# Performance work log

Hardware: AMD Instinct MI355X
Metric: run time of the kernel (lower is better)

The kernel has to match this reference:

```python
import jax, jax.numpy as jnp
import numpy as np

D = 256
EXP = 4


def layer_norm(x, gamma, beta, eps=1e-5):
    mu = jnp.mean(x, axis=-1, keepdims=True)
    var = jnp.var(x, axis=-1, keepdims=True)
    return (x - mu) / jnp.sqrt(var + eps) * gamma + beta


def setup_inputs() -> dict:
    key = jax.random.key(0)
    ks = jax.random.split(key, 7)
    B, N = 8, 2048
    x = jax.random.normal(ks[0], (B, N, D), dtype=jnp.float32)
    w1 = jax.random.normal(ks[1], (D, EXP * D), dtype=jnp.float32) * (1.0 / np.sqrt(D))
    b1 = jnp.zeros((EXP * D,), dtype=jnp.float32)
    w2 = jax.random.normal(ks[2], (EXP * D, D), dtype=jnp.float32) * (1.0 / np.sqrt(EXP * D))
    b2 = jnp.zeros((D,), dtype=jnp.float32)
    g1 = jnp.ones((D,), dtype=jnp.float32)
    be1 = jnp.zeros((D,), dtype=jnp.float32)
    g2 = jnp.ones((D,), dtype=jnp.float32)
    be2 = jnp.zeros((D,), dtype=jnp.float32)
    return {"x": x, "w1": w1, "b1": b1, "w2": w2, "b2": b2,
            "gamma1": g1, "beta1": be1, "gamma2": g2, "beta2": be2}


def reference(x, w1, b1, w2, b2, gamma1, beta1, gamma2, beta2):
    # Sublayer 1: x + SA(LN(x)); SA uses raw QK^T softmax with Q=K=V=LN(x)
    h = layer_norm(x, gamma1, beta1)               # [B,N,D]
    scale = jnp.sqrt(jnp.float32(h.shape[-1]))
    scores = jnp.einsum('bnd,bmd->bnm', h, h) / scale  # [B,N,N]
    prob = jax.nn.softmax(scores, axis=-1)
    sa_out = jnp.einsum('bnm,bmd->bnd', prob, h)
    x = x + sa_out
    # Sublayer 2: x + FFN(LN(x))
    h2 = layer_norm(x, gamma2, beta2)
    ffn = jax.nn.relu(h2 @ w1 + b1) @ w2 + b2
    return x + ffn
```

## Files before the change

kernel.cpp:

```cpp
#include <hip/hip_runtime.h>
#include <hip/hip_bf16.h>

typedef unsigned short u16;
typedef __attribute__((ext_vector_type(8))) short short8;
typedef __attribute__((ext_vector_type(4))) float f32x4;

typedef unsigned int __attribute__((address_space(1))) as1_u32;
typedef unsigned int __attribute__((address_space(3))) as3_u32;

__device__ __forceinline__ void gload16(const void* g, void* l) {
    __builtin_amdgcn_global_load_lds((const as1_u32*)g, (as3_u32*)l, 16, 0, 0);
}

__device__ __forceinline__ u16 f2b(float f) {
    union { float f; unsigned u; } v; v.f = f;
    unsigned r = v.u + 0x7fffu + ((v.u >> 16) & 1u);
    return (u16)(r >> 16);
}

__global__ void transpose_cast(const float* __restrict__ src,
                               u16* __restrict__ dst, int R, int C) {
    __shared__ float tile[32][33];
    const int c0 = blockIdx.x * 32, r0 = blockIdx.y * 32;
    const int tx = threadIdx.x, ty = threadIdx.y;
#pragma unroll
    for (int i = ty; i < 32; i += 8)
        tile[i][tx] = src[(size_t)(r0 + i) * C + c0 + tx];
    __syncthreads();
#pragma unroll
    for (int i = ty; i < 32; i += 8)
        dst[(size_t)(c0 + i) * R + r0 + tx] = f2b(tile[tx][i]);
}

__global__ void transpose_bf16(const u16* __restrict__ src, u16* __restrict__ dst) {
    __shared__ u16 t[32][33];
    const int b = blockIdx.z;
    const int n0 = blockIdx.x * 32, d0 = blockIdx.y * 32;
    const int tx = threadIdx.x, ty = threadIdx.y;
    const u16* s = src + (size_t)b * (2048 * 256);
    u16* d = dst + (size_t)b * (2048 * 256);
#pragma unroll
    for (int i = ty; i < 32; i += 8)
        t[i][tx] = s[(size_t)(n0 + i) * 256 + d0 + tx];
    __syncthreads();
#pragma unroll
    for (int i = ty; i < 32; i += 8)
        d[(size_t)(d0 + i) * 2048 + n0 + tx] = t[tx][i];
}

__global__ __launch_bounds__(256) void ln_kernel(
    const float* __restrict__ x, const float* __restrict__ g,
    const float* __restrict__ be, u16* __restrict__ out) {
    const int lane = threadIdx.x & 63;
    const size_t row = (size_t)blockIdx.x * 4 + (threadIdx.x >> 6);
    const float4 v = *((const float4*)(x + row * 256) + lane);
    float s  = v.x + v.y + v.z + v.w;
    float s2 = v.x * v.x + v.y * v.y + v.z * v.z + v.w * v.w;
#pragma unroll
    for (int m = 1; m < 64; m <<= 1) {
        s  += __shfl_xor(s, m);
        s2 += __shfl_xor(s2, m);
    }
    const float mean = s * (1.0f / 256.0f);
    const float var  = s2 * (1.0f / 256.0f) - mean * mean;
    const float rstd = rsqrtf(var + 1e-5f);
    const float4 gv = *((const float4*)g + lane);
    const float4 bv = *((const float4*)be + lane);
    ushort4 o;
    o.x = f2b((v.x - mean) * rstd * gv.x + bv.x);
    o.y = f2b((v.y - mean) * rstd * gv.y + bv.y);
    o.z = f2b((v.z - mean) * rstd * gv.z + bv.z);
    o.w = f2b((v.w - mean) * rstd * gv.w + bv.w);
    *((ushort4*)(out + row * 256) + lane) = o;
}

#define ATTN_LDS_BYTES (2*65536 + 4*16*72*2)

__global__ __launch_bounds__(256) void attn_kernel(
    const u16* __restrict__ h, const u16* __restrict__ hT,
    const float* __restrict__ x, float* __restrict__ xmid) {
    extern __shared__ char smem[];
    const int tid  = threadIdx.x;
    const int w    = tid >> 6;
    const int lane = tid & 63;
    const int grp  = lane >> 4;
    const int l16  = lane & 15;
    const int b    = blockIdx.y;
    const int q0   = blockIdx.x * 64;

    const u16* hb = h + (size_t)b * (2048 * 256);
    const char* hbB = (const char*)hb;
    const char* hTB = (const char*)(hT + (size_t)b * (2048 * 256));
    u16* myP = (u16*)(smem + 131072) + w * (16 * 72);

    short8 qf[8];
    {
        const u16* qp = hb + (size_t)(q0 + w * 16 + l16) * 256 + grp * 8;
#pragma unroll
        for (int kk = 0; kk < 8; ++kk) qf[kk] = *(const short8*)(qp + kk * 32);
    }

    f32x4 oacc[16];
#pragma unroll
    for (int n = 0; n < 16; ++n) oacc[n] = (f32x4){0.f, 0.f, 0.f, 0.f};
    float m_run[4] = {-1e30f, -1e30f, -1e30f, -1e30f};
    float l_run[4] = {0.f, 0.f, 0.f, 0.f};

    const char* gK0 = hbB + ((size_t)(tid >> 5) << 9)
                          + (((tid & 31) ^ (tid >> 5)) << 4);
    const char* gV0 = hTB + ((size_t)(tid >> 3) << 12)
                          + (((tid & 7) ^ ((tid >> 3) & 7)) << 4);

    {
        char* lK = smem + w * 1024;
        char* lV = smem + 32768 + w * 1024;
#pragma unroll
        for (int it = 0; it < 8; ++it) gload16(gK0 + (size_t)it * 4096, lK + it * 4096);
#pragma unroll
        for (int it = 0; it < 8; ++it) gload16(gV0 + (size_t)it * 131072, lV + it * 4096);
    }
    __syncthreads();

    for (int kt = 0; kt < 32; ++kt) {
        const int cur = kt & 1;
        if (kt < 31) {
            char* lK = smem + (cur ^ 1) * 65536 + w * 1024;
            char* lV = smem + (cur ^ 1) * 65536 + 32768 + w * 1024;
            const char* gK = gK0 + (size_t)(kt + 1) * 32768;
            const char* gV = gV0 + (size_t)(kt + 1) * 128;
#pragma unroll
            for (int it = 0; it < 8; ++it) gload16(gK + (size_t)it * 4096, lK + it * 4096);
#pragma unroll
            for (int it = 0; it < 8; ++it) gload16(gV + (size_t)it * 131072, lV + it * 4096);
        }
        const char* KBb = smem + cur * 65536;
        const char* VBb = KBb + 32768;

        f32x4 sacc[4];
#pragma unroll
        for (int j = 0; j < 4; ++j) sacc[j] = (f32x4){0.f, 0.f, 0.f, 0.f};
#pragma unroll
        for (int j = 0; j < 4; ++j) {
            const char* rb = KBb + ((j * 16 + l16) << 9);
#pragma unroll
            for (int kk = 0; kk < 8; ++kk) {
                const int c = grp + 4 * kk;
                const int swz = (c & ~7) | ((c ^ l16) & 7);
                sacc[j] = __builtin_amdgcn_mfma_f32_16x16x32_bf16(
                    qf[kk], *(const short8*)(rb + (swz << 4)), sacc[j], 0, 0, 0);
            }
        }

        float sv[4][4];
#pragma unroll
        for (int j = 0; j < 4; ++j)
#pragma unroll
            for (int r = 0; r < 4; ++r) sv[j][r] = sacc[j][r] * 0.0625f;
#pragma unroll
        for (int r = 0; r < 4; ++r) {
            float m = fmaxf(fmaxf(sv[0][r], sv[1][r]), fmaxf(sv[2][r], sv[3][r]));
            m = fmaxf(m, __shfl_xor(m, 1));
            m = fmaxf(m, __shfl_xor(m, 2));
            m = fmaxf(m, __shfl_xor(m, 4));
            m = fmaxf(m, __shfl_xor(m, 8));
            const float mnew  = fmaxf(m_run[r], m);
            const float alpha = __expf(m_run[r] - mnew);
            m_run[r] = mnew;
            float lt = 0.f;
#pragma unroll
            for (int j = 0; j < 4; ++j) {
                const float p = __expf(sv[j][r] - mnew);
                sv[j][r] = p;
                lt += p;
            }
            lt += __shfl_xor(lt, 1);
            lt += __shfl_xor(lt, 2);
            lt += __shfl_xor(lt, 4);
            lt += __shfl_xor(lt, 8);
            l_run[r] = l_run[r] * alpha + lt;
#pragma unroll
            for (int n = 0; n < 16; ++n) oacc[n][r] *= alpha;
#pragma unroll
            for (int j = 0; j < 4; ++j)
                myP[(grp * 4 + r) * 72 + j * 16 + l16] = f2b(sv[j][r]);
        }

#pragma unroll
        for (int kk2 = 0; kk2 < 2; ++kk2) {
            const short8 pa = *(const short8*)(myP + l16 * 72 + kk2 * 32 + grp * 8);
#pragma unroll
            for (int n = 0; n < 16; ++n) {
                const int cc2 = (4 * kk2 + grp) ^ (l16 & 7);
                oacc[n] = __builtin_amdgcn_mfma_f32_16x16x32_bf16(
                    pa, *(const short8*)(VBb + ((n * 16 + l16) << 7) + (cc2 << 4)),
                    oacc[n], 0, 0, 0);
            }
        }
        __syncthreads();
    }

    const float* xb = x + (size_t)b * (2048 * 256);
    float* ob = xmid + (size_t)b * (2048 * 256);
    float inv[4];
#pragma unroll
    for (int r = 0; r < 4; ++r) inv[r] = 1.0f / l_run[r];
#pragma unroll
    for (int n = 0; n < 16; ++n)
#pragma unroll
        for (int r = 0; r < 4; ++r) {
            const int row = q0 + w * 16 + grp * 4 + r;
            const int col = n * 16 + l16;
            const size_t idx = (size_t)row * 256 + col;
            ob[idx] = xb[idx] + oacc[n][r] * inv[r];
        }
}

#define FFN_LDS_BYTES (2*65536 + 4*16*72*2)

__global__ __launch_bounds__(256) void ffn_kernel(
    const u16* __restrict__ h2, const u16* __restrict__ w1t,
    const u16* __restrict__ w2t, const float* __restrict__ b1,
    const float* __restrict__ b2, float* __restrict__ xmid) {
    extern __shared__ char smem[];
    const int tid  = threadIdx.x;
    const int w    = tid >> 6;
    const int lane = tid & 63;
    const int grp  = lane >> 4;
    const int l16  = lane & 15;
    const int t0   = blockIdx.x * 64;
    u16* myA = (u16*)(smem + 131072) + w * (16 * 72);

    short8 af[8];
    {
        const u16* ap = h2 + (size_t)(t0 + w * 16 + l16) * 256 + grp * 8;
#pragma unroll
        for (int kk = 0; kk < 8; ++kk) af[kk] = *(const short8*)(ap + kk * 32);
    }

    f32x4 oacc[16];
#pragma unroll
    for (int n = 0; n < 16; ++n) oacc[n] = (f32x4){0.f, 0.f, 0.f, 0.f};

    const char* g10 = (const char*)w1t + ((size_t)(tid >> 5) << 9)
                                       + (((tid & 31) ^ (tid >> 5)) << 4);
    const char* g20 = (const char*)w2t + ((size_t)(tid >> 3) << 11)
                                       + (((tid & 7) ^ ((tid >> 3) & 7)) << 4);

    {
        char* l1 = smem + w * 1024;
        char* l2 = smem + 32768 + w * 1024;
#pragma unroll
        for (int it = 0; it < 8; ++it) gload16(g10 + (size_t)it * 4096, l1 + it * 4096);
#pragma unroll
        for (int it = 0; it < 8; ++it) gload16(g20 + (size_t)it * 65536, l2 + it * 4096);
    }
    __syncthreads();

    for (int hc = 0; hc < 16; ++hc) {
        const int cur = hc & 1;
        if (hc < 15) {
            char* l1 = smem + (cur ^ 1) * 65536 + w * 1024;
            char* l2 = smem + (cur ^ 1) * 65536 + 32768 + w * 1024;
            const char* g1 = g10 + (size_t)(hc + 1) * 32768;
            const char* g2 = g20 + (size_t)(hc + 1) * 128;
#pragma unroll
            for (int it = 0; it < 8; ++it) gload16(g1 + (size_t)it * 4096, l1 + it * 4096);
#pragma unroll
            for (int it = 0; it < 8; ++it) gload16(g2 + (size_t)it * 65536, l2 + it * 4096);
        }
        const char* W1b = smem + cur * 65536;
        const char* W2b = W1b + 32768;

        f32x4 sacc[4];
#pragma unroll
        for (int j = 0; j < 4; ++j) sacc[j] = (f32x4){0.f, 0.f, 0.f, 0.f};
#pragma unroll
        for (int j = 0; j < 4; ++j) {
            const char* rb = W1b + ((j * 16 + l16) << 9);
#pragma unroll
            for (int kk = 0; kk < 8; ++kk) {
                const int c = grp + 4 * kk;
                const int swz = (c & ~7) | ((c ^ l16) & 7);
                sacc[j] = __builtin_amdgcn_mfma_f32_16x16x32_bf16(
                    af[kk], *(const short8*)(rb + (swz << 4)), sacc[j], 0, 0, 0);
            }
        }

#pragma unroll
        for (int j = 0; j < 4; ++j) {
            const float bias = b1[hc * 64 + j * 16 + l16];
#pragma unroll
            for (int r = 0; r < 4; ++r) {
                float v = fmaxf(sacc[j][r] + bias, 0.f);
                myA[(grp * 4 + r) * 72 + j * 16 + l16] = f2b(v);
            }
        }

#pragma unroll
        for (int kk2 = 0; kk2 < 2; ++kk2) {
            const short8 pa = *(const short8*)(myA + l16 * 72 + kk2 * 32 + grp * 8);
#pragma unroll
            for (int n = 0; n < 16; ++n) {
                const int cc2 = (4 * kk2 + grp) ^ (l16 & 7);
                oacc[n] = __builtin_amdgcn_mfma_f32_16x16x32_bf16(
                    pa, *(const short8*)(W2b + ((n * 16 + l16) << 7) + (cc2 << 4)),
                    oacc[n], 0, 0, 0);
            }
        }
        __syncthreads();
    }

#pragma unroll
    for (int n = 0; n < 16; ++n) {
        const float bias2 = b2[n * 16 + l16];
#pragma unroll
        for (int r = 0; r < 4; ++r) {
            const int row = t0 + w * 16 + grp * 4 + r;
            const size_t idx = (size_t)row * 256 + n * 16 + l16;
            xmid[idx] = xmid[idx] + oacc[n][r] + bias2;
        }
    }
}

extern "C" void kernel_launch(void* const* d_in, const int* in_sizes, int n_in,
                              void* d_out, int out_size, void* d_ws, size_t ws_size,
                              hipStream_t stream) {
    (void)in_sizes; (void)n_in; (void)out_size; (void)ws_size;
    const float* x   = (const float*)d_in[0];
    const float* w1  = (const float*)d_in[1];
    const float* b1  = (const float*)d_in[2];
    const float* w2  = (const float*)d_in[3];
    const float* b2  = (const float*)d_in[4];
    const float* g1  = (const float*)d_in[5];
    const float* be1 = (const float*)d_in[6];
    const float* g2  = (const float*)d_in[7];
    const float* be2 = (const float*)d_in[8];
    float* out = (float*)d_out;

    char* ws = (char*)d_ws;
    u16* h   = (u16*)ws;
    u16* hT  = (u16*)(ws + 8388608);
    u16* w1t = (u16*)(ws + 16777216);
    u16* w2t = (u16*)(ws + 17301504);

    hipFuncSetAttribute((const void*)attn_kernel,
                        hipFuncAttributeMaxDynamicSharedMemorySize, ATTN_LDS_BYTES);
    hipFuncSetAttribute((const void*)ffn_kernel,
                        hipFuncAttributeMaxDynamicSharedMemorySize, FFN_LDS_BYTES);

    transpose_cast<<<dim3(32, 8), dim3(32, 8), 0, stream>>>(w1, w1t, 256, 1024);
    transpose_cast<<<dim3(8, 32), dim3(32, 8), 0, stream>>>(w2, w2t, 1024, 256);

    ln_kernel<<<4096, 256, 0, stream>>>(x, g1, be1, h);
    transpose_bf16<<<dim3(64, 8, 8), dim3(32, 8), 0, stream>>>(h, hT);
    attn_kernel<<<dim3(32, 8), 256, ATTN_LDS_BYTES, stream>>>(h, hT, x, out);

    ln_kernel<<<4096, 256, 0, stream>>>(out, g2, be2, h);
    ffn_kernel<<<256, 256, FFN_LDS_BYTES, stream>>>(h, w1t, w2t, b1, b2, out);
}
```

Measured before the change: 228.3 us.

## Split key/hidden tiles across 8 waves and merge partial accumulators in LDS

Both the attention and FFN kernels go from 4 to 8 waves per block. Each pair of waves shares one 16-row query tile and splits the 64-wide key (or hidden) chunk in half, so each wave does half the score/P·V work per iteration. The two partial accumulators, plus the softmax max and sum for attention, are combined at the end through LDS. Attention also adds a lazy rescale that only updates the running max when the new tile max exceeds it by more than 8, which cuts the per-iteration multiplies of the output accumulator. The aim is more latency hiding and occupancy on a grid of only 256 blocks, at the cost of a final LDS reduction and more register pressure per block.

```diff
diff --git a/kernel.cpp b/kernel.cpp
--- a/kernel.cpp
+++ b/kernel.cpp
@@ -74,9 +74,9 @@
     *((ushort4*)(out + row * 256) + lane) = o;
 }
 
-#define ATTN_LDS_BYTES (2*65536 + 4*16*72*2)
-
-__global__ __launch_bounds__(256) void attn_kernel(
+#define ATTN_LDS_BYTES (2*65536 + 8*16*40*2)
+
+__global__ __launch_bounds__(512) void attn_kernel(
     const u16* __restrict__ h, const u16* __restrict__ hT,
     const float* __restrict__ x, float* __restrict__ xmid) {
     extern __shared__ char smem[];
@@ -85,17 +85,19 @@
     const int lane = tid & 63;
     const int grp  = lane >> 4;
     const int l16  = lane & 15;
+    const int qsub = w & 3;
+    const int kh   = w >> 2;
     const int b    = blockIdx.y;
     const int q0   = blockIdx.x * 64;
 
     const u16* hb = h + (size_t)b * (2048 * 256);
     const char* hbB = (const char*)hb;
     const char* hTB = (const char*)(hT + (size_t)b * (2048 * 256));
-    u16* myP = (u16*)(smem + 131072) + w * (16 * 72);
+    u16* myP = (u16*)(smem + 131072) + w * (16 * 40);
 
     short8 qf[8];
     {
-        const u16* qp = hb + (size_t)(q0 + w * 16 + l16) * 256 + grp * 8;
+        const u16* qp = hb + (size_t)(q0 + qsub * 16 + l16) * 256 + grp * 8;
 #pragma unroll
         for (int kk = 0; kk < 8; ++kk) qf[kk] = *(const short8*)(qp + kk * 32);
     }
@@ -107,7 +109,7 @@
     float l_run[4] = {0.f, 0.f, 0.f, 0.f};
 
     const char* gK0 = hbB + ((size_t)(tid >> 5) << 9)
-                          + (((tid & 31) ^ (tid >> 5)) << 4);
+                          + (((tid & 31) ^ ((tid >> 5) & 7)) << 4);
     const char* gV0 = hTB + ((size_t)(tid >> 3) << 12)
                           + (((tid & 7) ^ ((tid >> 3) & 7)) << 4);
 
@@ -115,9 +117,9 @@
         char* lK = smem + w * 1024;
         char* lV = smem + 32768 + w * 1024;
 #pragma unroll
-        for (int it = 0; it < 8; ++it) gload16(gK0 + (size_t)it * 4096, lK + it * 4096);
-#pragma unroll
-        for (int it = 0; it < 8; ++it) gload16(gV0 + (size_t)it * 131072, lV + it * 4096);
+        for (int it = 0; it < 4; ++it) gload16(gK0 + (size_t)it * 8192, lK + it * 8192);
+#pragma unroll
+        for (int it = 0; it < 4; ++it) gload16(gV0 + (size_t)it * 262144, lV + it * 8192);
     }
     __syncthreads();
 
@@ -129,19 +131,19 @@
             const char* gK = gK0 + (size_t)(kt + 1) * 32768;
             const char* gV = gV0 + (size_t)(kt + 1) * 128;
 #pragma unroll
-            for (int it = 0; it < 8; ++it) gload16(gK + (size_t)it * 4096, lK + it * 4096);
-#pragma unroll
-            for (int it = 0; it < 8; ++it) gload16(gV + (size_t)it * 131072, lV + it * 4096);
+            for (int it = 0; it < 4; ++it) gload16(gK + (size_t)it * 8192, lK + it * 8192);
+#pragma unroll
+            for (int it = 0; it < 4; ++it) gload16(gV + (size_t)it * 262144, lV + it * 8192);
         }
         const char* KBb = smem + cur * 65536;
         const char* VBb = KBb + 32768;
 
-        f32x4 sacc[4];
-#pragma unroll
-        for (int j = 0; j < 4; ++j) sacc[j] = (f32x4){0.f, 0.f, 0.f, 0.f};
-#pragma unroll
-        for (int j = 0; j < 4; ++j) {
-            const char* rb = KBb + ((j * 16 + l16) << 9);
+        f32x4 sacc[2];
+#pragma unroll
+        for (int j = 0; j < 2; ++j) sacc[j] = (f32x4){0.f, 0.f, 0.f, 0.f};
+#pragma unroll
+        for (int j = 0; j < 2; ++j) {
+            const char* rb = KBb + ((kh * 32 + j * 16 + l16) << 9);
 #pragma unroll
             for (int kk = 0; kk < 8; ++kk) {
                 const int c = grp + 4 * kk;
@@ -151,73 +153,112 @@
             }
         }
 
-        float sv[4][4];
-#pragma unroll
-        for (int j = 0; j < 4; ++j)
+        float sv[2][4];
+#pragma unroll
+        for (int j = 0; j < 2; ++j)
 #pragma unroll
             for (int r = 0; r < 4; ++r) sv[j][r] = sacc[j][r] * 0.0625f;
+        float tmax[4];
 #pragma unroll
         for (int r = 0; r < 4; ++r) {
-            float m = fmaxf(fmaxf(sv[0][r], sv[1][r]), fmaxf(sv[2][r], sv[3][r]));
+            float m = fmaxf(sv[0][r], sv[1][r]);
             m = fmaxf(m, __shfl_xor(m, 1));
             m = fmaxf(m, __shfl_xor(m, 2));
             m = fmaxf(m, __shfl_xor(m, 4));
             m = fmaxf(m, __shfl_xor(m, 8));
-            const float mnew  = fmaxf(m_run[r], m);
-            const float alpha = __expf(m_run[r] - mnew);
-            m_run[r] = mnew;
+            tmax[r] = m;
+        }
+        const bool need = (tmax[0] > m_run[0] + 8.f) || (tmax[1] > m_run[1] + 8.f) ||
+                          (tmax[2] > m_run[2] + 8.f) || (tmax[3] > m_run[3] + 8.f);
+        if (__any(need)) {
+#pragma unroll
+            for (int r = 0; r < 4; ++r) {
+                const float mnew  = fmaxf(m_run[r], tmax[r]);
+                const float alpha = __expf(m_run[r] - mnew);
+                m_run[r] = mnew;
+                l_run[r] *= alpha;
+#pragma unroll
+                for (int n = 0; n < 16; ++n) oacc[n][r] *= alpha;
+            }
+        }
+#pragma unroll
+        for (int r = 0; r < 4; ++r) {
             float lt = 0.f;
 #pragma unroll
-            for (int j = 0; j < 4; ++j) {
-                const float p = __expf(sv[j][r] - mnew);
-                sv[j][r] = p;
+            for (int j = 0; j < 2; ++j) {
+                const float p = __expf(sv[j][r] - m_run[r]);
                 lt += p;
+                myP[(grp * 4 + r) * 40 + j * 16 + l16] = f2b(p);
             }
             lt += __shfl_xor(lt, 1);
             lt += __shfl_xor(lt, 2);
             lt += __shfl_xor(lt, 4);
             lt += __shfl_xor(lt, 8);
-            l_run[r] = l_run[r] * alpha + lt;
-#pragma unroll
-            for (int n = 0; n < 16; ++n) oacc[n][r] *= alpha;
-#pragma unroll
-            for (int j = 0; j < 4; ++j)
-                myP[(grp * 4 + r) * 72 + j * 16 + l16] = f2b(sv[j][r]);
-        }
-
-#pragma unroll
-        for (int kk2 = 0; kk2 < 2; ++kk2) {
-            const short8 pa = *(const short8*)(myP + l16 * 72 + kk2 * 32 + grp * 8);
+            l_run[r] += lt;
+        }
+
+        {
+            const short8 pa = *(const short8*)(myP + l16 * 40 + grp * 8);
+            const int cc2 = ((kh << 2) + grp) ^ (l16 & 7);
 #pragma unroll
             for (int n = 0; n < 16; ++n) {
-                const int cc2 = (4 * kk2 + grp) ^ (l16 & 7);
-                oacc[n] = __builtin_amdgcn_mfma_f32_16x16x32_bf16(
-                    pa, *(const short8*)(VBb + ((n * 16 + l16) << 7) + (cc2 << 4)),
-                    oacc[n], 0, 0, 0);
+                const short8 bv =
+                    *(const short8*)(VBb + ((n * 16 + l16) << 7) + (cc2 << 4));
+                oacc[n] = __builtin_amdgcn_mfma_f32_16x16x32_bf16(pa, bv, oacc[n], 0, 0, 0);
             }
         }
         __syncthreads();
     }
 
-    const float* xb = x + (size_t)b * (2048 * 256);
-    float* ob = xmid + (size_t)b * (2048 * 256);
-    float inv[4];
-#pragma unroll
-    for (int r = 0; r < 4; ++r) inv[r] = 1.0f / l_run[r];
-#pragma unroll
-    for (int n = 0; n < 16; ++n)
-#pragma unroll
-        for (int r = 0; r < 4; ++r) {
-            const int row = q0 + w * 16 + grp * 4 + r;
-            const int col = n * 16 + l16;
-            const size_t idx = (size_t)row * 256 + col;
-            ob[idx] = xb[idx] + oacc[n][r] * inv[r];
-        }
-}
-
-#define FFN_LDS_BYTES (2*65536 + 4*16*72*2)
-
-__global__ __launch_bounds__(256) void ffn_kernel(
+    const int pair = w & 3;
+    if (w >= 4) {
+#pragma unroll
+        for (int n = 0; n < 16; ++n)
+            *(f32x4*)(smem + pair * 16384 + (n * 16 + l16) * 64 + grp * 16) = oacc[n];
+        if (l16 == 0) {
+            float* mlp = (float*)(smem + 131072 + pair * 128);
+#pragma unroll
+            for (int r = 0; r < 4; ++r) {
+                mlp[(grp * 4 + r) * 2]     = m_run[r];
+                mlp[(grp * 4 + r) * 2 + 1] = l_run[r];
+            }
+        }
+    }
+    __syncthreads();
+    if (w < 4) {
+        float c0[4], c1[4];
+        {
+            const float* mlp = (const float*)(smem + 131072 + w * 128);
+#pragma unroll
+            for (int r = 0; r < 4; ++r) {
+                const float m1 = mlp[(grp * 4 + r) * 2];
+                const float l1 = mlp[(grp * 4 + r) * 2 + 1];
+                const float M  = fmaxf(m_run[r], m1);
+                const float a0 = __expf(m_run[r] - M);
+                const float a1 = __expf(m1 - M);
+                const float inv = 1.0f / (l_run[r] * a0 + l1 * a1);
+                c0[r] = a0 * inv;
+                c1[r] = a1 * inv;
+            }
+        }
+        const float* xb = x + (size_t)b * (2048 * 256);
+        float* ob = xmid + (size_t)b * (2048 * 256);
+#pragma unroll
+        for (int n = 0; n < 16; ++n) {
+            const f32x4 o1 = *(const f32x4*)(smem + w * 16384 + (n * 16 + l16) * 64 + grp * 16);
+#pragma unroll
+            for (int r = 0; r < 4; ++r) {
+                const int row = q0 + w * 16 + grp * 4 + r;
+                const size_t idx = (size_t)row * 256 + n * 16 + l16;
+                ob[idx] = xb[idx] + oacc[n][r] * c0[r] + o1[r] * c1[r];
+            }
+        }
+    }
+}
+
+#define FFN_LDS_BYTES (2*65536 + 8*16*40*2)
+
+__global__ __launch_bounds__(512) void ffn_kernel(
     const u16* __restrict__ h2, const u16* __restrict__ w1t,
     const u16* __restrict__ w2t, const float* __restrict__ b1,
     const float* __restrict__ b2, float* __restrict__ xmid) {
@@ -227,12 +268,14 @@
     const int lane = tid & 63;
     const int grp  = lane >> 4;
     const int l16  = lane & 15;
+    const int qsub = w & 3;
+    const int hh   = w >> 2;
     const int t0   = blockIdx.x * 64;
-    u16* myA = (u16*)(smem + 131072) + w * (16 * 72);
+    u16* myA = (u16*)(smem + 131072) + w * (16 * 40);
 
     short8 af[8];
     {
-        const u16* ap = h2 + (size_t)(t0 + w * 16 + l16) * 256 + grp * 8;
+        const u16* ap = h2 + (size_t)(t0 + qsub * 16 + l16) * 256 + grp * 8;
 #pragma unroll
         for (int kk = 0; kk < 8; ++kk) af[kk] = *(const short8*)(ap + kk * 32);
     }
@@ -242,7 +285,7 @@
     for (int n = 0; n < 16; ++n) oacc[n] = (f32x4){0.f, 0.f, 0.f, 0.f};
 
     const char* g10 = (const char*)w1t + ((size_t)(tid >> 5) << 9)
-                                       + (((tid & 31) ^ (tid >> 5)) << 4);
+                                       + (((tid & 31) ^ ((tid >> 5) & 7)) << 4);
     const char* g20 = (const char*)w2t + ((size_t)(tid >> 3) << 11)
                                        + (((tid & 7) ^ ((tid >> 3) & 7)) << 4);
 
@@ -250,9 +293,9 @@
         char* l1 = smem + w * 1024;
         char* l2 = smem + 32768 + w * 1024;
 #pragma unroll
-        for (int it = 0; it < 8; ++it) gload16(g10 + (size_t)it * 4096, l1 + it * 4096);
-#pragma unroll
-        for (int it = 0; it < 8; ++it) gload16(g20 + (size_t)it * 65536, l2 + it * 4096);
+        for (int it = 0; it < 4; ++it) gload16(g10 + (size_t)it * 8192, l1 + it * 8192);
+#pragma unroll
+        for (int it = 0; it < 4; ++it) gload16(g20 + (size_t)it * 131072, l2 + it * 8192);
     }
     __syncthreads();
 
@@ -264,19 +307,19 @@
             const char* g1 = g10 + (size_t)(hc + 1) * 32768;
             const char* g2 = g20 + (size_t)(hc + 1) * 128;
 #pragma unroll
-            for (int it = 0; it < 8; ++it) gload16(g1 + (size_t)it * 4096, l1 + it * 4096);
-#pragma unroll
-            for (int it = 0; it < 8; ++it) gload16(g2 + (size_t)it * 65536, l2 + it * 4096);
+            for (int it = 0; it < 4; ++it) gload16(g1 + (size_t)it * 8192, l1 + it * 8192);
+#pragma unroll
+            for (int it = 0; it < 4; ++it) gload16(g2 + (size_t)it * 131072, l2 + it * 8192);
         }
         const char* W1b = smem + cur * 65536;
         const char* W2b = W1b + 32768;
 
-        f32x4 sacc[4];
-#pragma unroll
-        for (int j = 0; j < 4; ++j) sacc[j] = (f32x4){0.f, 0.f, 0.f, 0.f};
-#pragma unroll
-        for (int j = 0; j < 4; ++j) {
-            const char* rb = W1b + ((j * 16 + l16) << 9);
+        f32x4 sacc[2];
+#pragma unroll
+        for (int j = 0; j < 2; ++j) sacc[j] = (f32x4){0.f, 0.f, 0.f, 0.f};
+#pragma unroll
+        for (int j = 0; j < 2; ++j) {
+            const char* rb = W1b + ((hh * 32 + j * 16 + l16) << 9);
 #pragma unroll
             for (int kk = 0; kk < 8; ++kk) {
                 const int c = grp + 4 * kk;
@@ -287,37 +330,46 @@
         }
 
 #pragma unroll
-        for (int j = 0; j < 4; ++j) {
-            const float bias = b1[hc * 64 + j * 16 + l16];
-#pragma unroll
-            for (int r = 0; r < 4; ++r) {
-                float v = fmaxf(sacc[j][r] + bias, 0.f);
-                myA[(grp * 4 + r) * 72 + j * 16 + l16] = f2b(v);
-            }
-        }
-
-#pragma unroll
-        for (int kk2 = 0; kk2 < 2; ++kk2) {
-            const short8 pa = *(const short8*)(myA + l16 * 72 + kk2 * 32 + grp * 8);
+        for (int j = 0; j < 2; ++j) {
+            const float bias = b1[hc * 64 + hh * 32 + j * 16 + l16];
+#pragma unroll
+            for (int r = 0; r < 4; ++r) {
+                const float v = fmaxf(sacc[j][r] + bias, 0.f);
+                myA[(grp * 4 + r) * 40 + j * 16 + l16] = f2b(v);
+            }
+        }
+
+        {
+            const short8 pa = *(const short8*)(myA + l16 * 40 + grp * 8);
+            const int cc2 = ((hh << 2) + grp) ^ (l16 & 7);
 #pragma unroll
             for (int n = 0; n < 16; ++n) {
-                const int cc2 = (4 * kk2 + grp) ^ (l16 & 7);
-                oacc[n] = __builtin_amdgcn_mfma_f32_16x16x32_bf16(
-                    pa, *(const short8*)(W2b + ((n * 16 + l16) << 7) + (cc2 << 4)),
-                    oacc[n], 0, 0, 0);
+                const short8 bv =
+                    *(const short8*)(W2b + ((n * 16 + l16) << 7) + (cc2 << 4));
+                oacc[n] = __builtin_amdgcn_mfma_f32_16x16x32_bf16(pa, bv, oacc[n], 0, 0, 0);
             }
         }
         __syncthreads();
     }
 
-#pragma unroll
-    for (int n = 0; n < 16; ++n) {
-        const float bias2 = b2[n * 16 + l16];
-#pragma unroll
-        for (int r = 0; r < 4; ++r) {
-            const int row = t0 + w * 16 + grp * 4 + r;
-            const size_t idx = (size_t)row * 256 + n * 16 + l16;
-            xmid[idx] = xmid[idx] + oacc[n][r] + bias2;
+    const int pair = w & 3;
+    if (w >= 4) {
+#pragma unroll
+        for (int n = 0; n < 16; ++n)
+            *(f32x4*)(smem + pair * 16384 + (n * 16 + l16) * 64 + grp * 16) = oacc[n];
+    }
+    __syncthreads();
+    if (w < 4) {
+#pragma unroll
+        for (int n = 0; n < 16; ++n) {
+            const f32x4 o1 = *(const f32x4*)(smem + w * 16384 + (n * 16 + l16) * 64 + grp * 16);
+            const float bias2 = b2[n * 16 + l16];
+#pragma unroll
+            for (int r = 0; r < 4; ++r) {
+                const int row = t0 + w * 16 + grp * 4 + r;
+                const size_t idx = (size_t)row * 256 + n * 16 + l16;
+                xmid[idx] = xmid[idx] + oacc[n][r] + o1[r] + bias2;
+            }
         }
     }
 }
@@ -353,8 +405,8 @@
 
     ln_kernel<<<4096, 256, 0, stream>>>(x, g1, be1, h);
     transpose_bf16<<<dim3(64, 8, 8), dim3(32, 8), 0, stream>>>(h, hT);
-    attn_kernel<<<dim3(32, 8), 256, ATTN_LDS_BYTES, stream>>>(h, hT, x, out);
+    attn_kernel<<<dim3(32, 8), 512, ATTN_LDS_BYTES, stream>>>(h, hT, x, out);
 
     ln_kernel<<<4096, 256, 0, stream>>>(out, g2, be2, h);
-    ffn_kernel<<<256, 256, FFN_LDS_BYTES, stream>>>(h, w1t, w2t, b1, b2, out);
-}
+    ffn_kernel<<<256, 512, FFN_LDS_BYTES, stream>>>(h, w1t, w2t, b1, b2, out);
+}
```

New measurement: 216.9 us. -5.0%, faster.
